# Optimization experiments

Hardware: AMD Instinct MI355X
Metric: run time of the kernel (lower is better)

## Reference

```python
import jax, jax.numpy as jnp
import numpy as np

BN_EPS = 1e-5
W_BITS = 2
A_BITS = 2


def _quantize_k(x, k):
    # uniform quantization of x in [0,1] to k bits, straight-through estimator
    n = float(2 ** k - 1)
    q = jnp.round(x * n) / n
    return x + jax.lax.stop_gradient(q - x)


def _quant_weight(w, k):
    # DoReFa-style weight quantization to [-1, 1]
    t = jnp.tanh(w)
    t = t / (2.0 * jnp.max(jnp.abs(t))) + 0.5
    return 2.0 * _quantize_k(t, k) - 1.0


def _quant_act(x, k):
    # DoReFa-style activation quantization: clamp to [0,1], quantize
    return _quantize_k(jnp.clip(x, 0.0, 1.0), k)


def _conv3x3(x, w, stride=1):
    # x: [N,C,H,W], w: [O,I,3,3], padding=1
    return jax.lax.conv_general_dilated(
        x, w, window_strides=(stride, stride), padding=((1, 1), (1, 1)),
        dimension_numbers=('NCHW', 'OIHW', 'NCHW'))


def _bn(x, gamma, beta, mean, var):
    inv = gamma / jnp.sqrt(var + BN_EPS)           # [C]
    return x * inv[None, :, None, None] + (beta - mean * inv)[None, :, None, None]


def setup_inputs() -> dict:
    key = jax.random.key(0)
    ks = jax.random.split(key, 8)
    N, C, H, W = 64, 256, 28, 28
    x = jax.random.normal(ks[0], (N, C, H, W), dtype=jnp.float32)
    w1 = jax.random.normal(ks[1], (C, C, 3, 3), dtype=jnp.float32) * 0.05
    w2 = jax.random.normal(ks[2], (C, C, 3, 3), dtype=jnp.float32) * 0.05
    g1 = jnp.ones((C,), jnp.float32)
    b1 = jnp.zeros((C,), jnp.float32)
    m1 = jax.random.normal(ks[3], (C,), dtype=jnp.float32) * 0.1
    v1 = jax.random.uniform(ks[4], (C,), dtype=jnp.float32) + 0.5
    g2 = jnp.ones((C,), jnp.float32)
    b2 = jnp.zeros((C,), jnp.float32)
    m2 = jax.random.normal(ks[5], (C,), dtype=jnp.float32) * 0.1
    v2 = jax.random.uniform(ks[6], (C,), dtype=jnp.float32) + 0.5
    return {'x': x, 'w1': w1, 'g1': g1, 'b1': b1, 'm1': m1, 'v1': v1,
            'w2': w2, 'g2': g2, 'b2': b2, 'm2': m2, 'v2': v2}


def reference(x, w1, g1, b1, m1, v1, w2, g2, b2, m2, v2):
    residual = x
    # conv1 (2-bit quantized weights & activations) -> bn1 -> relu
    out = _conv3x3(_quant_act(x, A_BITS), _quant_weight(w1, W_BITS), stride=1)
    out = jax.nn.relu(_bn(out, g1, b1, m1, v1))
    # conv2 (2-bit quantized) -> bn2
    out = _conv3x3(_quant_act(out, A_BITS), _quant_weight(w2, W_BITS), stride=1)
    out = _bn(out, g2, b2, m2, v2)
    # residual add + relu
    return jax.nn.relu(out + residual)
```

## Files before the change

### kernel.cpp

```cpp
#include <hip/hip_runtime.h>


#define ABUF 14745600
using i32x4 = __attribute__((ext_vector_type(4))) int;

__device__ __forceinline__ void gload16(const void* g, void* l) {
  typedef const __attribute__((address_space(1))) unsigned int* gp_t;
  typedef __attribute__((address_space(3))) unsigned int* lp_t;
  __builtin_amdgcn_global_load_lds((gp_t)g, (lp_t)l, 16, 0, 0);
}

__device__ __forceinline__ int border_pix(int bp) {
  int hh, ww;
  if (bp < 30)      { hh = 0;       ww = bp; }
  else if (bp < 60) { hh = 29;      ww = bp - 30; }
  else if (bp < 88) { hh = bp - 59; ww = 0; }
  else              { hh = bp - 87; ww = 29; }
  return hh * 30 + ww;
}

__global__ void pre_k(const float* __restrict__ x, unsigned char* __restrict__ a1,
                      unsigned char* __restrict__ a2,
                      const float* __restrict__ w1, const float* __restrict__ w2,
                      float* __restrict__ partial,
                      const float* g1, const float* b1, const float* m1, const float* v1,
                      const float* g2, const float* b2, const float* m2, const float* v2,
                      float* s1, float* t1, float* s2, float* t2) {
  const int t = threadIdx.x;
  if (blockIdx.x >= 256) {
    int bx = blockIdx.x - 256;
    int ten = bx >> 6, bxl = bx & 63;
    if (ten == 0 && bxl == 0) {
      float i1 = g1[t] / sqrtf(v1[t] + 1e-5f);
      s1[t] = i1 * (1.f / 9.f);
      t1[t] = b1[t] - m1[t] * i1;
      float i2 = g2[t] / sqrtf(v2[t] + 1e-5f);
      s2[t] = i2 * (1.f / 9.f);
      t2[t] = b2[t] - m2[t] * i2;
    }
    const float4* v = (const float4*)(ten ? w2 : w1);
    float loc = 0.f;
    for (int i = bxl * 256 + t; i < 147456; i += 16384) {
      float4 f = v[i];
      loc = fmaxf(loc, fmaxf(fmaxf(fabsf(f.x), fabsf(f.y)), fmaxf(fabsf(f.z), fabsf(f.w))));
    }
    #pragma unroll
    for (int off = 32; off; off >>= 1) loc = fmaxf(loc, __shfl_xor(loc, off));
    __shared__ float red[4];
    if ((t & 63) == 0) red[t >> 6] = loc;
    __syncthreads();
    if (t == 0)
      partial[ten * 64 + bxl] = fmaxf(fmaxf(red[0], red[1]), fmaxf(red[2], red[3]));
    return;
  }
  __shared__ unsigned au[784 * 17];
  const int n = blockIdx.x >> 2, cq = blockIdx.x & 3;
  const int c4 = t >> 4, q = t & 15;

  #pragma unroll
  for (int m = 0; m < 2; ++m) {
    int s2i = t + m * 256;
    if (s2i < 464) {
      int bp = s2i >> 2, quad = s2i & 3;
      size_t off = ((size_t)n * 900 + border_pix(bp)) * 256 + cq * 64 + quad * 16;
      uint4 z = {0, 0, 0, 0};
      *(uint4*)(a1 + off) = z;
      *(uint4*)(a2 + off) = z;
    }
  }

  const float* xb = x + (size_t)n * 200704 + (cq * 64 + c4 * 4) * 784;
  #pragma unroll
  for (int k = 0; k < 13; ++k) {
    int hw4 = q + k * 16;
    if (hw4 < 196) {
      unsigned b[4][4];
      #pragma unroll
      for (int i = 0; i < 4; ++i) {
        float4 f = *(const float4*)(xb + i * 784 + hw4 * 4);
        b[i][0] = (unsigned)(int)rintf(3.f * fminf(fmaxf(f.x, 0.f), 1.f));
        b[i][1] = (unsigned)(int)rintf(3.f * fminf(fmaxf(f.y, 0.f), 1.f));
        b[i][2] = (unsigned)(int)rintf(3.f * fminf(fmaxf(f.z, 0.f), 1.f));
        b[i][3] = (unsigned)(int)rintf(3.f * fminf(fmaxf(f.w, 0.f), 1.f));
      }
      #pragma unroll
      for (int j = 0; j < 4; ++j)
        au[(hw4 * 4 + j) * 17 + c4] = b[0][j] | (b[1][j] << 8) | (b[2][j] << 16) | (b[3][j] << 24);
    }
  }
  __syncthreads();
  #pragma unroll
  for (int m = 0; m < 13; ++m) {
    int s = t + m * 256;
    if (s < 3136) {
      int pix = s >> 2, quad = s & 3;
      uint4 v;
      v.x = au[pix * 17 + quad * 4 + 0];
      v.y = au[pix * 17 + quad * 4 + 1];
      v.z = au[pix * 17 + quad * 4 + 2];
      v.w = au[pix * 17 + quad * 4 + 3];
      int hh = pix / 28, ww = pix - hh * 28;
      *(uint4*)(a1 + (((n * 30 + hh + 1) * 30) + ww + 1) * 256 + cq * 64 + quad * 16) = v;
    }
  }
}

__global__ void wquant_k(const float* __restrict__ w1, const float* __restrict__ w2,
                         const float* __restrict__ partial,
                         signed char* __restrict__ wq1, signed char* __restrict__ wq2) {
  const int oo = blockIdx.x, ten = blockIdx.y;
  const float* w = ten ? w2 : w1;
  signed char* o = ten ? wq2 : wq1;
  __shared__ float wl[2304];
  const int t = threadIdx.x;
  float pm = partial[ten * 64 + (t & 63)];
  #pragma unroll
  for (int off = 32; off; off >>= 1) pm = fmaxf(pm, __shfl_xor(pm, off));
  const float inv = 1.f / (2.f * tanhf(pm));
  #pragma unroll
  for (int k = 0; k < 9; ++k) wl[k * 256 + t] = tanhf(w[oo * 2304 + k * 256 + t]);
  __syncthreads();
  #pragma unroll
  for (int k = 0; k < 9; ++k) {
    int j = k * 256 + t, t9 = j >> 8, ci = j & 255;
    float tt = wl[ci * 9 + t9] * inv + 0.5f;
    int q = (int)rintf(tt * 3.f);
    o[oo * 2304 + j] = (signed char)(2 * q - 3);
  }
}

#define PH_MID() do { __builtin_amdgcn_s_barrier(); \
  asm volatile("s_waitcnt lgkmcnt(0)" ::: "memory"); \
  __builtin_amdgcn_sched_barrier(0); \
  __builtin_amdgcn_s_setprio(1); } while (0)
#define PH_END() do { __builtin_amdgcn_s_setprio(0); \
  __builtin_amdgcn_s_barrier(); } while (0)
#define PH_ENDV(N) do { __builtin_amdgcn_s_setprio(0); \
  asm volatile("s_waitcnt vmcnt(" #N ")" ::: "memory"); \
  __builtin_amdgcn_sched_barrier(0); \
  __builtin_amdgcn_s_barrier(); } while (0)

template <int MODE>
__global__ __launch_bounds__(512, 2) void conv_gemm(
    const unsigned char* __restrict__ act, const signed char* __restrict__ wq,
    const float* __restrict__ sC, const float* __restrict__ tC,
    const float* __restrict__ xres, unsigned char* __restrict__ actout,
    float* __restrict__ fout) {
  extern __shared__ __align__(16) char lds[];
  const int tid = threadIdx.x, wv = tid >> 6, lane = tid & 63;
  const int bswz = blockIdx.x & 7, bloc = blockIdx.x >> 3;
  const int wg = (bswz < 4 ? bswz * 25 : 100 + (bswz - 4) * 24) + bloc;
  const int pixBase = wg * 256;
  const int wvm = wv >> 2, wvn = wv & 3;
  constexpr int RAoff = (MODE == 0) ? 0 : 32768;
  constexpr int RBoff = 32768 - RAoff;

  int pixB[2][2], wB[2][2];
  {
    int s = (lane & 7) ^ ((lane >> 3) & 7);
    #pragma unroll
    for (int h = 0; h < 2; ++h)
      #pragma unroll
      for (int c = 0; c < 2; ++c) {
        int r = h * 128 + c * 64 + wv * 8 + (lane >> 3);
        int p = pixBase + r;
        int n = p / 784, rem = p % 784, hh = rem / 28, ww = rem % 28;
        pixB[h][c] = (((n * 30 + hh) * 30 + ww) << 8) + (s << 4);
        wB[h][c] = r * 2304 + (s << 4);
      }
  }
  auto tof = [](int kt) {
    int tap = kt >> 1;
    return ((tap / 3) * 30 + (tap % 3)) * 256 + ((kt & 1) << 7);
  };
  auto stagePix = [&](int h, int kt) {
    const int base = (kt & 1) * 65536 + h * 16384 + wv * 1024;
    const int toff = tof(kt);
    gload16(act + pixB[h][0] + toff, &lds[base]);
    gload16(act + pixB[h][1] + toff, &lds[base + 8192]);
  };
  auto stageW = [&](int h, int kt) {
    const int base = (kt & 1) * 65536 + 32768 + h * 16384 + wv * 1024;
    gload16(wq + wB[h][0] + kt * 128, &lds[base]);
    gload16(wq + wB[h][1] + kt * 128, &lds[base + 8192]);
  };
  auto stageA = [&](int h, int kt) { if (MODE == 0) stagePix(h, kt); else stageW(h, kt); };
  auto stageB = [&](int h, int kt) { if (MODE == 0) stageW(h, kt); else stagePix(h, kt); };

  i32x4 acc[8][4];
  #pragma unroll
  for (int i = 0; i < 8; ++i)
    #pragma unroll
    for (int j = 0; j < 4; ++j) acc[i][j] = (i32x4){0, 0, 0, 0};
  i32x4 pa[4][2], pb0[2][2], pb1[2][2];

  auto rdA = [&](int buf, int mh) {
    #pragma unroll
    for (int f = 0; f < 4; ++f) {
      int r = wvm * 128 + mh * 64 + f * 16 + (lane & 15);
      int rb = buf * 65536 + RAoff + r * 128;
      #pragma unroll
      for (int kc = 0; kc < 2; ++kc) {
        int sl = kc * 4 + (lane >> 4);
        pa[f][kc] = *(const i32x4*)&lds[rb + ((sl ^ (r & 7)) << 4)];
      }
    }
  };
  auto rdB = [&](int buf, int nh, i32x4 (*pb)[2]) {
    #pragma unroll
    for (int g = 0; g < 2; ++g) {
      int r = wvn * 64 + nh * 32 + g * 16 + (lane & 15);
      int rb = buf * 65536 + RBoff + r * 128;
      #pragma unroll
      for (int kc = 0; kc < 2; ++kc) {
        int sl = kc * 4 + (lane >> 4);
        pb[g][kc] = *(const i32x4*)&lds[rb + ((sl ^ (r & 7)) << 4)];
      }
    }
  };
  auto quad = [&](int mh, int nh, i32x4 (*pb)[2]) {
    #pragma unroll
    for (int kc = 0; kc < 2; ++kc)
      #pragma unroll
      for (int f = 0; f < 4; ++f)
        #pragma unroll
        for (int g = 0; g < 2; ++g)
          acc[mh * 4 + f][nh * 2 + g] = __builtin_amdgcn_mfma_i32_16x16x64_i8(
              pa[f][kc], pb[g][kc], acc[mh * 4 + f][nh * 2 + g], 0, 0, 0);
  };

  stageB(0, 0); stageA(0, 0); stageB(1, 0); stageA(1, 0);
  stageB(0, 1); stageA(0, 1); stageB(1, 1);
  asm volatile("s_waitcnt vmcnt(6)" ::: "memory");
  __builtin_amdgcn_sched_barrier(0);
  __builtin_amdgcn_s_barrier();

  for (int it = 0; it < 9; ++it) {
    const int ktY = 2 * it + 1, ktX2 = 2 * it + 2, ktY2 = 2 * it + 3;
    const bool st = (it < 8);
    rdA(0, 0); rdB(0, 0, pb0);
    stageA(1, ktY);
    PH_MID(); quad(0, 0, pb0); PH_END();
    rdB(0, 1, pb1);
    PH_MID(); quad(0, 1, pb1); PH_END();
    rdA(0, 1);
    if (st) stageB(0, ktX2);
    PH_MID(); quad(1, 0, pb0); PH_END();
    if (st) { stageA(0, ktX2); stageB(1, ktX2); }
    PH_MID(); quad(1, 1, pb1);
    if (st) { PH_ENDV(6); } else { PH_ENDV(0); }
    rdA(1, 0); rdB(1, 0, pb0);
    if (st) stageA(1, ktX2);
    PH_MID(); quad(0, 0, pb0); PH_END();
    rdB(1, 1, pb1);
    PH_MID(); quad(0, 1, pb1); PH_END();
    rdA(1, 1);
    if (st) stageB(0, ktY2);
    PH_MID(); quad(1, 0, pb0); PH_END();
    if (st) { stageA(0, ktY2); stageB(1, ktY2); }
    PH_MID(); quad(1, 1, pb1);
    PH_ENDV(6);
  }

  if (MODE == 0) {
    float sj[4], tj[4];
    #pragma unroll
    for (int j = 0; j < 4; ++j) {
      int c = wvn * 64 + j * 16 + (lane & 15);
      sj[j] = sC[c]; tj[j] = tC[c];
    }
    __syncthreads();
    #pragma unroll
    for (int i = 0; i < 8; ++i) {
      int lp0 = wvm * 128 + i * 16 + ((lane >> 4) << 2);
      #pragma unroll
      for (int j = 0; j < 4; ++j) {
        int lch = wvn * 64 + j * 16 + (lane & 15);
        #pragma unroll
        for (int r = 0; r < 4; ++r) {
          float y = (float)acc[i][j][r] * sj[j] + tj[j];
          y = fminf(fmaxf(y, 0.f), 1.f);
          int lp = lp0 + r;
          lds[lp * 256 + (lch ^ ((lp & 7) << 4))] = (char)(int)rintf(y * 3.f);
        }
      }
    }
    __syncthreads();
    int rr = tid >> 1, hf = tid & 1;
    int p = pixBase + rr;
    int n = p / 784, rem = p % 784, hh = rem / 28, ww = rem % 28;
    unsigned char* dst = actout + (((n * 30 + hh + 1) * 30 + (ww + 1)) << 8) + hf * 128;
    #pragma unroll
    for (int k = 0; k < 8; ++k) {
      uint4 v = *(const uint4*)&lds[rr * 256 + ((hf * 128 + k * 16) ^ ((rr & 7) << 4))];
      *(uint4*)(dst + k * 16) = v;
    }
  } else {
    #pragma unroll
    for (int i = 0; i < 8; ++i) {
      int c = wvm * 128 + i * 16 + ((lane >> 4) << 2) + (lane & 3);
      float sc = sC[c], tc = tC[c];
      #pragma unroll
      for (int j = 0; j < 4; ++j) {
        int a0 = acc[i][j][0], a1 = acc[i][j][1], a2 = acc[i][j][2], a3 = acc[i][j][3];
        int t0 = __builtin_amdgcn_mov_dpp(a0, 0xB1, 0xF, 0xF, true);
        int t1 = __builtin_amdgcn_mov_dpp(a1, 0xB1, 0xF, 0xF, true);
        int t2 = __builtin_amdgcn_mov_dpp(a2, 0xB1, 0xF, 0xF, true);
        int t3 = __builtin_amdgcn_mov_dpp(a3, 0xB1, 0xF, 0xF, true);
        const bool o1 = (lane & 1) != 0;
        int v0 = o1 ? t1 : a0;
        int v1 = o1 ? a1 : t0;
        int v2 = o1 ? t3 : a2;
        int v3 = o1 ? a3 : t2;
        int u0 = __builtin_amdgcn_mov_dpp(v2, 0x4E, 0xF, 0xF, true);
        int u1 = __builtin_amdgcn_mov_dpp(v3, 0x4E, 0xF, 0xF, true);
        int u2 = __builtin_amdgcn_mov_dpp(v0, 0x4E, 0xF, 0xF, true);
        int u3 = __builtin_amdgcn_mov_dpp(v1, 0x4E, 0xF, 0xF, true);
        const bool o2 = (lane & 2) != 0;
        int z0 = o2 ? u0 : v0;
        int z1 = o2 ? u1 : v1;
        int z2 = o2 ? v2 : u2;
        int z3 = o2 ? v3 : u3;
        int P = pixBase + wvn * 64 + j * 16 + (lane & 12);
        int n = P / 784, rem = P - n * 784;
        size_t addr = (size_t)n * 200704 + (size_t)c * 784 + rem;
        float4 xr = *(const float4*)(xres + addr);
        float4 y;
        y.x = fmaxf((float)z0 * sc + tc + xr.x, 0.f);
        y.y = fmaxf((float)z1 * sc + tc + xr.y, 0.f);
        y.z = fmaxf((float)z2 * sc + tc + xr.z, 0.f);
        y.w = fmaxf((float)z3 * sc + tc + xr.w, 0.f);
        *(float4*)(fout + addr) = y;
      }
    }
  }
}

extern "C" void kernel_launch(void* const* d_in, const int* in_sizes, int n_in,
                              void* d_out, int out_size, void* d_ws, size_t ws_size,
                              hipStream_t stream) {
  const float* x  = (const float*)d_in[0];
  const float* w1 = (const float*)d_in[1];
  const float* g1 = (const float*)d_in[2];
  const float* b1 = (const float*)d_in[3];
  const float* m1 = (const float*)d_in[4];
  const float* v1 = (const float*)d_in[5];
  const float* w2 = (const float*)d_in[6];
  const float* g2 = (const float*)d_in[7];
  const float* b2 = (const float*)d_in[8];
  const float* m2 = (const float*)d_in[9];
  const float* v2 = (const float*)d_in[10];

  char* ws = (char*)d_ws;
  float* partial = (float*)ws;
  float* s1 = (float*)(ws + 1024);
  float* t1 = (float*)(ws + 2048);
  float* s2 = (float*)(ws + 3072);
  float* t2 = (float*)(ws + 4096);
  unsigned char* a1 = (unsigned char*)(ws + 8192);
  unsigned char* a2 = a1 + ABUF;
  signed char* wq1 = (signed char*)(a2 + ABUF);
  signed char* wq2 = wq1 + 589824;

  void (*k0)(const unsigned char*, const signed char*, const float*, const float*,
             const float*, unsigned char*, float*) = conv_gemm<0>;
  void (*k1)(const unsigned char*, const signed char*, const float*, const float*,
             const float*, unsigned char*, float*) = conv_gemm<1>;
  hipFuncSetAttribute((const void*)k0, hipFuncAttributeMaxDynamicSharedMemorySize, 131072);
  hipFuncSetAttribute((const void*)k1, hipFuncAttributeMaxDynamicSharedMemorySize, 131072);

  pre_k<<<384, 256, 0, stream>>>(x, a1, a2, w1, w2, partial,
                                 g1, b1, m1, v1, g2, b2, m2, v2, s1, t1, s2, t2);
  wquant_k<<<dim3(256, 2), 256, 0, stream>>>(w1, w2, partial, wq1, wq2);
  conv_gemm<0><<<196, 512, 131072, stream>>>(a1, wq1, s1, t1, nullptr, a2, nullptr);
  conv_gemm<1><<<196, 512, 131072, stream>>>(a2, wq2, s2, t2, x, nullptr, (float*)d_out);
}
```

Measured before the change: 204.6 us.

## Replace ping-pong phase barriers with per-tile double-buffered pipeline in conv GEMM

Restructures the main K-loop of the int8 MFMA conv GEMM. The old loop interleaved eight barrier-separated phases per two k-tiles. The new loop processes one k-tile per iteration with a single block barrier, staging the full tile two steps ahead and using lgkmcnt waits to overlap LDS reads with MFMA. The aim is to cut barrier and setprio synchronisation overhead. The trade-off is a full vmcnt(0) drain each iteration, which may expose global-load latency.

```diff
diff --git a/kernel.cpp b/kernel.cpp
--- a/kernel.cpp
+++ b/kernel.cpp
@@ -129,16 +129,9 @@
   }
 }
 
-#define PH_MID() do { __builtin_amdgcn_s_barrier(); \
-  asm volatile("s_waitcnt lgkmcnt(0)" ::: "memory"); \
-  __builtin_amdgcn_sched_barrier(0); \
-  __builtin_amdgcn_s_setprio(1); } while (0)
-#define PH_END() do { __builtin_amdgcn_s_setprio(0); \
-  __builtin_amdgcn_s_barrier(); } while (0)
-#define PH_ENDV(N) do { __builtin_amdgcn_s_setprio(0); \
-  asm volatile("s_waitcnt vmcnt(" #N ")" ::: "memory"); \
-  __builtin_amdgcn_sched_barrier(0); \
-  __builtin_amdgcn_s_barrier(); } while (0)
+#define LGKM(N) do { asm volatile("s_waitcnt lgkmcnt(" #N ")" ::: "memory"); \
+  __builtin_amdgcn_sched_barrier(0); } while (0)
+#define SBAR0() __builtin_amdgcn_sched_barrier(0)
 
 template <int MODE>
 __global__ __launch_bounds__(512, 2) void conv_gemm(
@@ -184,8 +177,10 @@
     gload16(wq + wB[h][0] + kt * 128, &lds[base]);
     gload16(wq + wB[h][1] + kt * 128, &lds[base + 8192]);
   };
-  auto stageA = [&](int h, int kt) { if (MODE == 0) stagePix(h, kt); else stageW(h, kt); };
-  auto stageB = [&](int h, int kt) { if (MODE == 0) stageW(h, kt); else stagePix(h, kt); };
+  auto stageT = [&](int kt) {
+    if (MODE == 0) { stagePix(0, kt); stagePix(1, kt); stageW(0, kt); stageW(1, kt); }
+    else           { stageW(0, kt); stageW(1, kt); stagePix(0, kt); stagePix(1, kt); }
+  };
 
   i32x4 acc[8][4];
   #pragma unroll
@@ -229,37 +224,34 @@
               pa[f][kc], pb[g][kc], acc[mh * 4 + f][nh * 2 + g], 0, 0, 0);
   };
 
-  stageB(0, 0); stageA(0, 0); stageB(1, 0); stageA(1, 0);
-  stageB(0, 1); stageA(0, 1); stageB(1, 1);
-  asm volatile("s_waitcnt vmcnt(6)" ::: "memory");
-  __builtin_amdgcn_sched_barrier(0);
+  stageT(0); stageT(1);
+  asm volatile("s_waitcnt vmcnt(8)" ::: "memory");
+  SBAR0();
   __builtin_amdgcn_s_barrier();
-
-  for (int it = 0; it < 9; ++it) {
-    const int ktY = 2 * it + 1, ktX2 = 2 * it + 2, ktY2 = 2 * it + 3;
-    const bool st = (it < 8);
-    rdA(0, 0); rdB(0, 0, pb0);
-    stageA(1, ktY);
-    PH_MID(); quad(0, 0, pb0); PH_END();
-    rdB(0, 1, pb1);
-    PH_MID(); quad(0, 1, pb1); PH_END();
-    rdA(0, 1);
-    if (st) stageB(0, ktX2);
-    PH_MID(); quad(1, 0, pb0); PH_END();
-    if (st) { stageA(0, ktX2); stageB(1, ktX2); }
-    PH_MID(); quad(1, 1, pb1);
-    if (st) { PH_ENDV(6); } else { PH_ENDV(0); }
-    rdA(1, 0); rdB(1, 0, pb0);
-    if (st) stageA(1, ktX2);
-    PH_MID(); quad(0, 0, pb0); PH_END();
-    rdB(1, 1, pb1);
-    PH_MID(); quad(0, 1, pb1); PH_END();
-    rdA(1, 1);
-    if (st) stageB(0, ktY2);
-    PH_MID(); quad(1, 0, pb0); PH_END();
-    if (st) { stageA(0, ktY2); stageB(1, ktY2); }
-    PH_MID(); quad(1, 1, pb1);
-    PH_ENDV(6);
+  asm volatile("" ::: "memory");
+
+  for (int t = 0; t < 18; ++t) {
+    const int buf = t & 1;
+    rdA(buf, 0); rdB(buf, 0, pb0);
+    SBAR0();
+    rdB(buf, 1, pb1);
+    LGKM(4);
+    __builtin_amdgcn_s_setprio(1); quad(0, 0, pb0); __builtin_amdgcn_s_setprio(0);
+    LGKM(0);
+    __builtin_amdgcn_s_setprio(1); quad(0, 1, pb1); __builtin_amdgcn_s_setprio(0);
+    rdA(buf, 1);
+    if (t < 17) {
+      asm volatile("s_waitcnt vmcnt(0) lgkmcnt(0)" ::: "memory");
+      SBAR0();
+      __builtin_amdgcn_s_barrier();
+      asm volatile("" ::: "memory");
+      if (t < 16) stageT(t + 2);
+    } else {
+      LGKM(0);
+    }
+    __builtin_amdgcn_s_setprio(1);
+    quad(1, 0, pb0); quad(1, 1, pb1);
+    __builtin_amdgcn_s_setprio(0);
   }
 
   if (MODE == 0) {
```

After: 198.1 us. 3.2% less time.
